# Kernel optimization log

Measured on AMD Instinct MI355X. Metric: run time of the kernel, lower is better.

## Reference

```python
import jax, jax.numpy as jnp
import numpy as np

COST_CLASS, COST_MASK, COST_DICE = 2.0, 5.0, 5.0
NUM_POINTS = 12544

def setup_inputs() -> dict:
    key = jax.random.key(0)
    k1, k2, k3, k4, k5 = jax.random.split(key, 5)
    bs, Q, K = 4, 100, 134
    H = W = 256
    M = 80
    P = H * W
    pred_logits = jax.random.normal(k1, (bs, Q, K), dtype=jnp.float32)
    pred_masks = jax.random.normal(k2, (bs, Q, H, W), dtype=jnp.float32)
    tgt_labels = jax.random.randint(k3, (M,), 0, K - 1, dtype=jnp.int32)
    # binary target masks, stored as float (matches .float() in torch code)
    tgt_masks = (jax.random.uniform(k4, (M, H, W)) > 0.5).astype(jnp.float32)
    # random subset of points without replacement (torch.randperm[:num_points])
    point_idx = jax.random.permutation(k5, P)[:NUM_POINTS].astype(jnp.int32)
    return {"pred_logits": pred_logits, "pred_masks": pred_masks,
            "tgt_labels": tgt_labels, "tgt_masks": tgt_masks,
            "point_idx": point_idx}

def reference(pred_logits, pred_masks, tgt_labels, tgt_masks, point_idx):
    bs, Q, K = pred_logits.shape
    N = bs * Q
    M = tgt_masks.shape[0]
    Pn = point_idx.shape[0]

    # class cost: -p[n, tgt_id[m]]
    out_prob = jax.nn.softmax(pred_logits.reshape(N, K), axis=-1)
    tgt_ids = jnp.clip(tgt_labels.astype(jnp.int32), 0, K - 1)
    cost_class = -out_prob[:, tgt_ids]                      # (N, M)

    # sampled mask logits / targets
    x = pred_masks.reshape(N, -1)[:, point_idx]             # (N, Pn) logits
    y = tgt_masks.reshape(M, -1)[:, point_idx]              # (M, Pn) binary float

    # BCE-with-logits cost, separable form:
    # mean_p[softplus(x) - x*y] = mean_p softplus(x) - (x @ y^T)/Pn
    sp_mean = jnp.mean(jax.nn.softplus(x), axis=-1)         # (N,)
    xy = jnp.einsum('np,mp->nm', x, y)                      # (N, M)
    cost_mask = sp_mean[:, None] - xy / Pn

    # dice cost
    s = jax.nn.sigmoid(x)                                   # (N, Pn)
    numer = 2.0 * jnp.einsum('np,mp->nm', s, y)             # (N, M)
    denom = jnp.sum(s, axis=-1)[:, None] + jnp.sum(y, axis=-1)[None, :]
    cost_dice = 1.0 - (numer + 1.0) / (denom + 1.0)

    C = COST_CLASS * cost_class + COST_MASK * cost_mask + COST_DICE * cost_dice
    return C.reshape(bs, Q, M)
```

## Files before the change

kernel.cpp:

```cpp
#include <hip/hip_runtime.h>
#include <math.h>

#define N_ROWS 400
#define M_ROWS 80
#define K_CLS  134
#define PN     12544
#define PFULL  65536
#define NSUB   25
#define TSTEPS 392
#define KSPLIT 56
#define TPB    7

#define GX_BLOCKS 400
#define GY_BLOCKS 245
#define SM_BLOCKS 50

typedef __attribute__((ext_vector_type(4))) float  f32x4;
typedef __attribute__((ext_vector_type(8))) __bf16 bf16x8;
typedef __attribute__((ext_vector_type(4))) __bf16 bf16x4;

__device__ __forceinline__ float wave_reduce_sum(float v) {
#pragma unroll
    for (int off = 32; off > 0; off >>= 1) v += __shfl_down(v, off, 64);
    return v;
}

__global__ __launch_bounds__(1024) void sel_sort_kernel(
        const int* __restrict__ point_idx, int* __restrict__ sel,
        float* __restrict__ zero_region, int zero_n) {
    __shared__ unsigned int flagw[PFULL / 4];
    __shared__ int wtot[16], wbase[16];
    int tid = threadIdx.x;
    for (int i = tid; i < PFULL / 4; i += 1024) flagw[i] = 0u;
    for (int i = tid; i < zero_n; i += 1024) zero_region[i] = 0.f;
    __syncthreads();
    unsigned char* flag = (unsigned char*)flagw;
    for (int i = tid; i < PN; i += 1024) flag[point_idx[i]] = 1;
    __syncthreads();
    unsigned int w[16];
    int cnt = 0;
#pragma unroll
    for (int j = 0; j < 16; ++j) {
        w[j] = flagw[tid * 16 + j];
        cnt += (int)((w[j] * 0x01010101u) >> 24);
    }
    int lane = tid & 63, wid = tid >> 6;
    int v = cnt;
#pragma unroll
    for (int off = 1; off < 64; off <<= 1) {
        int u = __shfl_up(v, off, 64);
        if (lane >= off) v += u;
    }
    if (lane == 63) wtot[wid] = v;
    __syncthreads();
    if (tid == 0) {
        int run = 0;
#pragma unroll
        for (int i = 0; i < 16; ++i) { wbase[i] = run; run += wtot[i]; }
    }
    __syncthreads();
    int base = wbase[wid] + (v - cnt);
#pragma unroll
    for (int j = 0; j < 16; ++j) {
        unsigned int u = w[j];
        int p0 = tid * 64 + j * 4;
        if (u & 0x01u)       sel[base++] = p0;
        if (u & 0x0100u)     sel[base++] = p0 + 1;
        if (u & 0x010000u)   sel[base++] = p0 + 2;
        if (u & 0x01000000u) sel[base++] = p0 + 3;
    }
}

__global__ __launch_bounds__(512) void stage1_kernel(
        const float* __restrict__ pred_masks, const float* __restrict__ tgt_masks,
        const float* __restrict__ pred_logits, const int* __restrict__ sel,
        __bf16* __restrict__ Xb, __bf16* __restrict__ Sb, __bf16* __restrict__ Yb,
        float* __restrict__ spsum, float* __restrict__ ssum, float* __restrict__ ysum,
        float* __restrict__ rowmax, float* __restrict__ rowsum) {
    __shared__ float smem[128];
    int b = blockIdx.x;
    if (b < GX_BLOCKS) {
        int n = b;
        const float* row = pred_masks + (size_t)n * PFULL;
        __bf16* xr = Xb + (size_t)n * PN;
        __bf16* sr = Sb + (size_t)n * PN;
        float ssp = 0.f, sss = 0.f;
#pragma unroll
        for (int it = 0; it < 7; ++it) {
            int k0 = it * 2048 + (int)threadIdx.x * 4;
            if (k0 < PN) {
                int4 id = *(const int4*)(sel + k0);
                float xs0 = row[id.x], xs1 = row[id.y], xs2 = row[id.z], xs3 = row[id.w];
                float xs[4] = {xs0, xs1, xs2, xs3};
                bf16x4 vx, vs;
#pragma unroll
                for (int q = 0; q < 4; ++q) {
                    float x  = xs[q];
                    float ax = fabsf(x);
                    float e  = __expf(-ax);
                    float inv = __builtin_amdgcn_rcpf(1.f + e);
                    float sig = (x >= 0.f) ? inv : e * inv;
                    float sp  = fmaxf(x, 0.f) + __logf(1.f + e);
                    vx[q] = (__bf16)x; vs[q] = (__bf16)sig;
                    ssp += sp; sss += sig;
                }
                *(bf16x4*)(xr + k0) = vx;
                *(bf16x4*)(sr + k0) = vs;
            }
        }
        float w1 = wave_reduce_sum(ssp), w2 = wave_reduce_sum(sss);
        int lane = threadIdx.x & 63, wid = threadIdx.x >> 6;
        if (lane == 0) { smem[wid] = w1; smem[8 + wid] = w2; }
        __syncthreads();
        if (threadIdx.x == 0) {
            float a = 0.f, c = 0.f;
#pragma unroll
            for (int i = 0; i < 8; ++i) { a += smem[i]; c += smem[8 + i]; }
            spsum[n] = a; ssum[n] = c;
        }
    } else if (b < GX_BLOCKS + GY_BLOCKS) {
        int bb = b - GX_BLOCKS;
        int j = bb / 49, tch = bb % 49;
        int wave = threadIdx.x >> 6, lane = threadIdx.x & 63;
        int colL = lane & 15, quad = lane >> 4;
        int m = 16 * j + colL;
        int t = tch * 8 + wave;
        int k0 = t * 32 + quad * 8;
        const float* yrow = tgt_masks + (size_t)m * PFULL;
        int idx[8];
        *(int4*)(idx)     = *(const int4*)(sel + k0);
        *(int4*)(idx + 4) = *(const int4*)(sel + k0 + 4);
        bf16x8 v; float acc = 0.f;
#pragma unroll
        for (int jj = 0; jj < 8; ++jj) {
            float y = yrow[idx[jj]];
            v[jj] = (__bf16)y;
            acc += y;
        }
        ((bf16x8*)Yb)[(size_t)(t * 5 + j) * 64 + lane] = v;
        acc += __shfl_down(acc, 32, 64);
        acc += __shfl_down(acc, 16, 64);
        if (quad == 0) smem[wave * 16 + colL] = acc;
        __syncthreads();
        if (threadIdx.x < 16) {
            float s = 0.f;
#pragma unroll
            for (int wv = 0; wv < 8; ++wv) s += smem[wv * 16 + threadIdx.x];
            atomicAdd(&ysum[16 * j + threadIdx.x], s);
        }
    } else {
        int bb = b - GX_BLOCKS - GY_BLOCKS;
        int wave = threadIdx.x >> 6, lane = threadIdx.x & 63;
        int n = bb * 8 + wave;
        const float* row = pred_logits + n * K_CLS;
        float mx = -1e30f;
        for (int k = lane; k < K_CLS; k += 64) mx = fmaxf(mx, row[k]);
#pragma unroll
        for (int off = 32; off > 0; off >>= 1) mx = fmaxf(mx, __shfl_down(mx, off, 64));
        mx = __shfl(mx, 0, 64);
        float se = 0.f;
        for (int k = lane; k < K_CLS; k += 64) se += expf(row[k] - mx);
        se = wave_reduce_sum(se);
        if (lane == 0) { rowmax[n] = mx; rowsum[n] = se; }
    }
}

__global__ __launch_bounds__(256) void mfma_gemm_kernel(
        const __bf16* __restrict__ Xb, const __bf16* __restrict__ Sb,
        const __bf16* __restrict__ Yb,
        float* __restrict__ xyacc, float* __restrict__ syacc) {
    int wave = threadIdx.x >> 6, lane = threadIdx.x & 63;
    int nsub = blockIdx.x * 4 + wave;
    int nclamp = nsub < NSUB ? nsub : NSUB - 1;
    int n0 = nclamp * 16;
    int colL = lane & 15, quad = lane >> 4;
    int tbase = blockIdx.y * TPB;

    const __bf16* xrow = Xb + (size_t)(n0 + colL) * PN;
    const __bf16* srow = Sb + (size_t)(n0 + colL) * PN;
    const bf16x8* Yfrag = (const bf16x8*)Yb;

    f32x4 accX[5], accS[5];
    f32x4 zero = {0.f, 0.f, 0.f, 0.f};
#pragma unroll
    for (int j = 0; j < 5; ++j) { accX[j] = zero; accS[j] = zero; }

    bf16x8 Abuf[2], Sbuf[2], Bbuf[2][5];
    auto load = [&](int i, int bb) {
        int t = tbase + i;
        size_t ko = (size_t)t * 32 + quad * 8;
        Abuf[bb] = *(const bf16x8*)(xrow + ko);
        Sbuf[bb] = *(const bf16x8*)(srow + ko);
        const bf16x8* q = Yfrag + (size_t)(t * 5) * 64 + lane;
#pragma unroll
        for (int j = 0; j < 5; ++j) Bbuf[bb][j] = q[(size_t)j * 64];
    };

    load(0, 0);
#pragma unroll
    for (int i = 0; i < TPB; ++i) {
        int bb = i & 1;
        if (i + 1 < TPB) load(i + 1, bb ^ 1);
#pragma unroll
        for (int j = 0; j < 5; ++j) {
            accX[j] = __builtin_amdgcn_mfma_f32_16x16x32_bf16(Abuf[bb], Bbuf[bb][j], accX[j], 0, 0, 0);
            accS[j] = __builtin_amdgcn_mfma_f32_16x16x32_bf16(Sbuf[bb], Bbuf[bb][j], accS[j], 0, 0, 0);
        }
    }

    if (nsub < NSUB) {
#pragma unroll
        for (int j = 0; j < 5; ++j)
#pragma unroll
            for (int r = 0; r < 4; ++r) {
                int n = n0 + quad * 4 + r;
                int m = 16 * j + colL;
                atomicAdd(&xyacc[n * M_ROWS + m], accX[j][r]);
                atomicAdd(&syacc[n * M_ROWS + m], accS[j][r]);
            }
    }
}

__global__ void combine_kernel(const float* __restrict__ logits,
                               const int* __restrict__ tgt_labels,
                               const float* __restrict__ rowmax,
                               const float* __restrict__ rowsum,
                               const float* __restrict__ spsum,
                               const float* __restrict__ ssum,
                               const float* __restrict__ ysum,
                               const float* __restrict__ xyacc,
                               const float* __restrict__ syacc,
                               float* __restrict__ out) {
    int idx = blockIdx.x * blockDim.x + threadIdx.x;
    if (idx >= N_ROWS * M_ROWS) return;
    int n = idx / M_ROWS, m = idx % M_ROWS;
    int tid = tgt_labels[m];
    tid = min(max(tid, 0), K_CLS - 1);
    float p = expf(logits[n * K_CLS + tid] - rowmax[n]) / rowsum[n];
    float cost_class = -p;
    float cost_mask = (spsum[n] - xyacc[idx]) * (1.0f / PN);
    float cost_dice = 1.f - (2.f * syacc[idx] + 1.f) / (ssum[n] + ysum[m] + 1.f);
    out[idx] = 2.f * cost_class + 5.f * cost_mask + 5.f * cost_dice;
}

extern "C" void kernel_launch(void* const* d_in, const int* in_sizes, int n_in,
                              void* d_out, int out_size, void* d_ws, size_t ws_size,
                              hipStream_t stream) {
    const float* pred_logits = (const float*)d_in[0];
    const float* pred_masks  = (const float*)d_in[1];
    const int*   tgt_labels  = (const int*)d_in[2];
    const float* tgt_masks   = (const float*)d_in[3];
    const int*   point_idx   = (const int*)d_in[4];
    float* out = (float*)d_out;

    char* ws = (char*)d_ws;
    size_t off = 0;
    auto carve = [&](size_t nbytes) {
        char* p = ws + off;
        off += (nbytes + 255) & ~(size_t)255;
        return p;
    };
    float* xyacc = (float*)carve((size_t)N_ROWS * M_ROWS * 4);
    float* syacc = (float*)carve((size_t)N_ROWS * M_ROWS * 4);
    float* ysum  = (float*)carve(M_ROWS * 4);
    int zero_n = (int)(off / 4);
    int*   sel    = (int*)carve(PN * 4);
    float* spsum  = (float*)carve(N_ROWS * 4);
    float* ssum   = (float*)carve(N_ROWS * 4);
    float* rowmax = (float*)carve(N_ROWS * 4);
    float* rowsum = (float*)carve(N_ROWS * 4);
    __bf16* Xb = (__bf16*)carve((size_t)N_ROWS * PN * 2);
    __bf16* Sb = (__bf16*)carve((size_t)N_ROWS * PN * 2);
    __bf16* Yb = (__bf16*)carve((size_t)TSTEPS * 5 * 1024);
    (void)ws_size; (void)in_sizes; (void)n_in; (void)out_size;

    sel_sort_kernel<<<1, 1024, 0, stream>>>(point_idx, sel, xyacc, zero_n);
    stage1_kernel<<<GX_BLOCKS + GY_BLOCKS + SM_BLOCKS, 512, 0, stream>>>(
        pred_masks, tgt_masks, pred_logits, sel, Xb, Sb, Yb,
        spsum, ssum, ysum, rowmax, rowsum);
    dim3 grid((NSUB + 3) / 4, KSPLIT);
    mfma_gemm_kernel<<<grid, 256, 0, stream>>>(Xb, Sb, Yb, xyacc, syacc);
    combine_kernel<<<(N_ROWS * M_ROWS + 255) / 256, 256, 0, stream>>>(
        pred_logits, tgt_labels, rowmax, rowsum, spsum, ssum, ysum, xyacc, syacc, out);
}
```

Baseline: 222.6 us.

## Fuse pred-mask gather and sigmoid/softplus into the MFMA GEMM kernel

The X/S bf16 intermediate buffers and the pred_masks gather blocks of stage1 are removed. The GEMM waves now gather pred_masks values through the sorted point index, compute sigmoid and softplus in registers, and feed the MFMAs directly. Row sums of sigmoid and softplus are accumulated with atomics. The K split is changed to 98 chunks of 4 steps, with a flat wave index and no padded waves. This saves the write and reread of about 20 MB of intermediates, at the cost of scattered fp32 gathers inside the GEMM loop and more atomics.

```diff
diff --git a/kernel.cpp b/kernel.cpp
--- a/kernel.cpp
+++ b/kernel.cpp
@@ -8,16 +8,14 @@
 #define PFULL  65536
 #define NSUB   25
 #define TSTEPS 392
-#define KSPLIT 56
-#define TPB    7
-
-#define GX_BLOCKS 400
+#define KSPLIT 98
+#define TPB    4
+
 #define GY_BLOCKS 245
 #define SM_BLOCKS 50
 
 typedef __attribute__((ext_vector_type(4))) float  f32x4;
 typedef __attribute__((ext_vector_type(8))) __bf16 bf16x8;
-typedef __attribute__((ext_vector_type(4))) __bf16 bf16x4;
 
 __device__ __forceinline__ float wave_reduce_sum(float v) {
 #pragma unroll
@@ -71,56 +69,14 @@
     }
 }
 
-__global__ __launch_bounds__(512) void stage1_kernel(
-        const float* __restrict__ pred_masks, const float* __restrict__ tgt_masks,
-        const float* __restrict__ pred_logits, const int* __restrict__ sel,
-        __bf16* __restrict__ Xb, __bf16* __restrict__ Sb, __bf16* __restrict__ Yb,
-        float* __restrict__ spsum, float* __restrict__ ssum, float* __restrict__ ysum,
-        float* __restrict__ rowmax, float* __restrict__ rowsum) {
+__global__ __launch_bounds__(512) void stage1b_kernel(
+        const float* __restrict__ tgt_masks, const float* __restrict__ pred_logits,
+        const int* __restrict__ sel, __bf16* __restrict__ Yb,
+        float* __restrict__ ysum, float* __restrict__ rowmax, float* __restrict__ rowsum) {
     __shared__ float smem[128];
     int b = blockIdx.x;
-    if (b < GX_BLOCKS) {
-        int n = b;
-        const float* row = pred_masks + (size_t)n * PFULL;
-        __bf16* xr = Xb + (size_t)n * PN;
-        __bf16* sr = Sb + (size_t)n * PN;
-        float ssp = 0.f, sss = 0.f;
-#pragma unroll
-        for (int it = 0; it < 7; ++it) {
-            int k0 = it * 2048 + (int)threadIdx.x * 4;
-            if (k0 < PN) {
-                int4 id = *(const int4*)(sel + k0);
-                float xs0 = row[id.x], xs1 = row[id.y], xs2 = row[id.z], xs3 = row[id.w];
-                float xs[4] = {xs0, xs1, xs2, xs3};
-                bf16x4 vx, vs;
-#pragma unroll
-                for (int q = 0; q < 4; ++q) {
-                    float x  = xs[q];
-                    float ax = fabsf(x);
-                    float e  = __expf(-ax);
-                    float inv = __builtin_amdgcn_rcpf(1.f + e);
-                    float sig = (x >= 0.f) ? inv : e * inv;
-                    float sp  = fmaxf(x, 0.f) + __logf(1.f + e);
-                    vx[q] = (__bf16)x; vs[q] = (__bf16)sig;
-                    ssp += sp; sss += sig;
-                }
-                *(bf16x4*)(xr + k0) = vx;
-                *(bf16x4*)(sr + k0) = vs;
-            }
-        }
-        float w1 = wave_reduce_sum(ssp), w2 = wave_reduce_sum(sss);
-        int lane = threadIdx.x & 63, wid = threadIdx.x >> 6;
-        if (lane == 0) { smem[wid] = w1; smem[8 + wid] = w2; }
-        __syncthreads();
-        if (threadIdx.x == 0) {
-            float a = 0.f, c = 0.f;
-#pragma unroll
-            for (int i = 0; i < 8; ++i) { a += smem[i]; c += smem[8 + i]; }
-            spsum[n] = a; ssum[n] = c;
-        }
-    } else if (b < GX_BLOCKS + GY_BLOCKS) {
-        int bb = b - GX_BLOCKS;
-        int j = bb / 49, tch = bb % 49;
+    if (b < GY_BLOCKS) {
+        int j = b / 49, tch = b % 49;
         int wave = threadIdx.x >> 6, lane = threadIdx.x & 63;
         int colL = lane & 15, quad = lane >> 4;
         int m = 16 * j + colL;
@@ -149,7 +105,7 @@
             atomicAdd(&ysum[16 * j + threadIdx.x], s);
         }
     } else {
-        int bb = b - GX_BLOCKS - GY_BLOCKS;
+        int bb = b - GY_BLOCKS;
         int wave = threadIdx.x >> 6, lane = threadIdx.x & 63;
         int n = bb * 8 + wave;
         const float* row = pred_logits + n * K_CLS;
@@ -165,59 +121,86 @@
     }
 }
 
-__global__ __launch_bounds__(256) void mfma_gemm_kernel(
-        const __bf16* __restrict__ Xb, const __bf16* __restrict__ Sb,
+__global__ __launch_bounds__(256) void gemm_fused_kernel(
+        const float* __restrict__ pred_masks, const int* __restrict__ sel,
         const __bf16* __restrict__ Yb,
-        float* __restrict__ xyacc, float* __restrict__ syacc) {
+        float* __restrict__ xyacc, float* __restrict__ syacc,
+        float* __restrict__ spsum, float* __restrict__ ssum) {
     int wave = threadIdx.x >> 6, lane = threadIdx.x & 63;
-    int nsub = blockIdx.x * 4 + wave;
-    int nclamp = nsub < NSUB ? nsub : NSUB - 1;
-    int n0 = nclamp * 16;
+    int flat = blockIdx.x * 4 + wave;
+    if (flat >= NSUB * KSPLIT) return;
+    int nsub = flat / KSPLIT, kc = flat % KSPLIT;
+    int n0 = nsub * 16;
     int colL = lane & 15, quad = lane >> 4;
-    int tbase = blockIdx.y * TPB;
-
-    const __bf16* xrow = Xb + (size_t)(n0 + colL) * PN;
-    const __bf16* srow = Sb + (size_t)(n0 + colL) * PN;
+    int tbase = kc * TPB;
+
+    const float* row = pred_masks + (size_t)(n0 + colL) * PFULL;
     const bf16x8* Yfrag = (const bf16x8*)Yb;
 
     f32x4 accX[5], accS[5];
     f32x4 zero = {0.f, 0.f, 0.f, 0.f};
 #pragma unroll
     for (int j = 0; j < 5; ++j) { accX[j] = zero; accS[j] = zero; }
-
-    bf16x8 Abuf[2], Sbuf[2], Bbuf[2][5];
-    auto load = [&](int i, int bb) {
+    float sumS = 0.f, sumSP = 0.f;
+
+    float xs[2][8];
+    bf16x8 Bbuf[2][5];
+    auto load = [&](int i, int b) {
         int t = tbase + i;
-        size_t ko = (size_t)t * 32 + quad * 8;
-        Abuf[bb] = *(const bf16x8*)(xrow + ko);
-        Sbuf[bb] = *(const bf16x8*)(srow + ko);
+        int k0 = t * 32 + quad * 8;
+        int idx[8];
+        *(int4*)(idx)     = *(const int4*)(sel + k0);
+        *(int4*)(idx + 4) = *(const int4*)(sel + k0 + 4);
+#pragma unroll
+        for (int jj = 0; jj < 8; ++jj) xs[b][jj] = row[idx[jj]];
         const bf16x8* q = Yfrag + (size_t)(t * 5) * 64 + lane;
 #pragma unroll
-        for (int j = 0; j < 5; ++j) Bbuf[bb][j] = q[(size_t)j * 64];
+        for (int j = 0; j < 5; ++j) Bbuf[b][j] = q[(size_t)j * 64];
     };
+    auto process = [&](int b) {
+        bf16x8 aX, aS;
+#pragma unroll
+        for (int jj = 0; jj < 8; ++jj) {
+            float x  = xs[b][jj];
+            float ax = fabsf(x);
+            float e  = __expf(-ax);
+            float inv = __builtin_amdgcn_rcpf(1.f + e);
+            float sig = (x >= 0.f) ? inv : e * inv;
+            float sp  = fmaxf(x, 0.f) + __logf(1.f + e);
+            aX[jj] = (__bf16)x; aS[jj] = (__bf16)sig;
+            sumS += sig; sumSP += sp;
+        }
+#pragma unroll
+        for (int j = 0; j < 5; ++j) {
+            accX[j] = __builtin_amdgcn_mfma_f32_16x16x32_bf16(aX, Bbuf[b][j], accX[j], 0, 0, 0);
+            accS[j] = __builtin_amdgcn_mfma_f32_16x16x32_bf16(aS, Bbuf[b][j], accS[j], 0, 0, 0);
+        }
+    };
 
     load(0, 0);
 #pragma unroll
     for (int i = 0; i < TPB; ++i) {
-        int bb = i & 1;
-        if (i + 1 < TPB) load(i + 1, bb ^ 1);
-#pragma unroll
-        for (int j = 0; j < 5; ++j) {
-            accX[j] = __builtin_amdgcn_mfma_f32_16x16x32_bf16(Abuf[bb], Bbuf[bb][j], accX[j], 0, 0, 0);
-            accS[j] = __builtin_amdgcn_mfma_f32_16x16x32_bf16(Sbuf[bb], Bbuf[bb][j], accS[j], 0, 0, 0);
-        }
-    }
-
-    if (nsub < NSUB) {
-#pragma unroll
-        for (int j = 0; j < 5; ++j)
-#pragma unroll
-            for (int r = 0; r < 4; ++r) {
-                int n = n0 + quad * 4 + r;
-                int m = 16 * j + colL;
-                atomicAdd(&xyacc[n * M_ROWS + m], accX[j][r]);
-                atomicAdd(&syacc[n * M_ROWS + m], accS[j][r]);
-            }
+        int b = i & 1;
+        if (i + 1 < TPB) load(i + 1, b ^ 1);
+        process(b);
+    }
+
+#pragma unroll
+    for (int j = 0; j < 5; ++j)
+#pragma unroll
+        for (int r = 0; r < 4; ++r) {
+            int n = n0 + quad * 4 + r;
+            int m = 16 * j + colL;
+            atomicAdd(&xyacc[n * M_ROWS + m], accX[j][r]);
+            atomicAdd(&syacc[n * M_ROWS + m], accS[j][r]);
+        }
+    sumS  += __shfl_down(sumS, 32, 64);
+    sumS  += __shfl_down(sumS, 16, 64);
+    sumSP += __shfl_down(sumSP, 32, 64);
+    sumSP += __shfl_down(sumSP, 16, 64);
+    if (lane < 16) {
+        atomicAdd(&ssum[n0 + lane], sumS);
+        atomicAdd(&spsum[n0 + lane], sumSP);
     }
 }
 
@@ -263,23 +246,21 @@
     float* xyacc = (float*)carve((size_t)N_ROWS * M_ROWS * 4);
     float* syacc = (float*)carve((size_t)N_ROWS * M_ROWS * 4);
     float* ysum  = (float*)carve(M_ROWS * 4);
+    float* spsum = (float*)carve(N_ROWS * 4);
+    float* ssum  = (float*)carve(N_ROWS * 4);
     int zero_n = (int)(off / 4);
     int*   sel    = (int*)carve(PN * 4);
-    float* spsum  = (float*)carve(N_ROWS * 4);
-    float* ssum   = (float*)carve(N_ROWS * 4);
     float* rowmax = (float*)carve(N_ROWS * 4);
     float* rowsum = (float*)carve(N_ROWS * 4);
-    __bf16* Xb = (__bf16*)carve((size_t)N_ROWS * PN * 2);
-    __bf16* Sb = (__bf16*)carve((size_t)N_ROWS * PN * 2);
     __bf16* Yb = (__bf16*)carve((size_t)TSTEPS * 5 * 1024);
     (void)ws_size; (void)in_sizes; (void)n_in; (void)out_size;
 
     sel_sort_kernel<<<1, 1024, 0, stream>>>(point_idx, sel, xyacc, zero_n);
-    stage1_kernel<<<GX_BLOCKS + GY_BLOCKS + SM_BLOCKS, 512, 0, stream>>>(
-        pred_masks, tgt_masks, pred_logits, sel, Xb, Sb, Yb,
-        spsum, ssum, ysum, rowmax, rowsum);
-    dim3 grid((NSUB + 3) / 4, KSPLIT);
-    mfma_gemm_kernel<<<grid, 256, 0, stream>>>(Xb, Sb, Yb, xyacc, syacc);
+    stage1b_kernel<<<GY_BLOCKS + SM_BLOCKS, 512, 0, stream>>>(
+        tgt_masks, pred_logits, sel, Yb, ysum, rowmax, rowsum);
+    int nwaves = NSUB * KSPLIT;
+    gemm_fused_kernel<<<(nwaves + 3) / 4, 256, 0, stream>>>(
+        pred_masks, sel, Yb, xyacc, syacc, spsum, ssum);
     combine_kernel<<<(N_ROWS * M_ROWS + 255) / 256, 256, 0, stream>>>(
         pred_logits, tgt_labels, rowmax, rowsum, spsum, ssum, ysum, xyacc, syacc, out);
 }
```

Measured after the change: 217.7 us. -2.2%, faster.
